# Performance work log

Measured on AMD Instinct MI355X. Metric: run time of the kernel, lower is better.

## Reference

```python
import jax, jax.numpy as jnp
import numpy as np

K = 512   # codebook entries per group (num_embeddings // 4)
D = 128   # dim per group (embedding_dim // 4)
BETA = 0.25


def setup_inputs() -> dict:
    key = jax.random.key(0)
    k0, k1, k2, k3, k4 = jax.random.split(key, 5)
    latents = jax.random.normal(k0, (16, 2048, 512), dtype=jnp.float32)
    scale = 1.0 / K
    w1 = jax.random.uniform(k1, (K, D), dtype=jnp.float32, minval=-scale, maxval=scale)
    w2 = jax.random.uniform(k2, (K, D), dtype=jnp.float32, minval=-scale, maxval=scale)
    w3 = jax.random.uniform(k3, (K, D), dtype=jnp.float32, minval=-scale, maxval=scale)
    w4 = jax.random.uniform(k4, (K, D), dtype=jnp.float32, minval=-scale, maxval=scale)
    return {"latents": latents, "w1": w1, "w2": w2, "w3": w3, "w4": w4}


def _vq(latents, w1, w2, w3, w4):
    B, S, E = latents.shape
    # Slicing [:, :, g*D:(g+1)*D] is equivalent to reshape into groups.
    x = latents.reshape(B, S, 4, D)                    # [B,S,4,D]
    W = jnp.stack([w1, w2, w3, w4], axis=0)            # [4,K,D]
    x_sq = jnp.sum(x * x, axis=-1, keepdims=True)      # [B,S,4,1]
    w_sq = jnp.sum(W * W, axis=-1)                     # [4,K]
    cross = jnp.einsum('bsgd,gkd->bsgk', x, W)         # [B,S,4,K]
    dist = x_sq + w_sq[None, None, :, :] - 2.0 * cross
    idx = jnp.argmin(dist, axis=-1)                    # [B,S,4]
    g_idx = jnp.arange(4)[None, None, :]
    q = W[g_idx, idx]                                  # [B,S,4,D]
    # per-group MSE losses (mean over B,S,D)
    sg = jax.lax.stop_gradient
    commit = jnp.mean((sg(q) - x) ** 2, axis=(0, 1, 3))   # [4]
    embed = jnp.mean((q - sg(x)) ** 2, axis=(0, 1, 3))    # [4]
    vq_loss = jnp.sum(BETA * commit + embed)
    # straight-through estimator
    q_st = x + sg(q - x)
    return q_st.reshape(B, S, E), vq_loss


def reference(latents, w1, w2, w3, w4):
    return _vq(latents, w1, w2, w3, w4)
```

## Files before the change

### kernel.cpp

```cpp
#include <hip/hip_runtime.h>
#include <stdint.h>

typedef __attribute__((ext_vector_type(8))) short short8;
typedef __attribute__((ext_vector_type(4))) float f32x4;

#define BIG 4.0f

static __device__ __forceinline__ short f2bf(float f) {
    union { float f; uint32_t u; } v; v.f = f;
    uint32_t u = v.u;
    return (short)((u + 0x7FFFu + ((u >> 16) & 1u)) >> 16);
}

static __device__ __forceinline__ void gload_lds16(const void* g, void* l) {
    __builtin_amdgcn_global_load_lds(
        (const __attribute__((address_space(1))) unsigned int*)g,
        (__attribute__((address_space(3))) unsigned int*)l, 16, 0, 0);
}


__global__ void vq_prep_kernel(const float* __restrict__ w0, const float* __restrict__ w1,
                               const float* __restrict__ w2, const float* __restrict__ w3,
                               float* __restrict__ ws) {
    int tid = blockIdx.x * 256 + threadIdx.x;
    int code = tid >> 4;
    int u    = tid & 15;
    int g = code >> 9, c = code & 511;
    int nt = c >> 4, lr = c & 15, ks = u >> 2, lh = u & 3;
    const float* wg = (g == 0) ? w0 : (g == 1) ? w1 : (g == 2) ? w2 : w3;
    const float* src = wg + (size_t)c * 128 + u * 8;
    float4 v0 = *(const float4*)(src);
    float4 v1 = *(const float4*)(src + 4);
    float s = v0.x*v0.x + v0.y*v0.y + v0.z*v0.z + v0.w*v0.w
            + v1.x*v1.x + v1.y*v1.y + v1.z*v1.z + v1.w*v1.w;
    short8 b;
    b[0] = f2bf(v0.x); b[1] = f2bf(v0.y); b[2] = f2bf(v0.z); b[3] = f2bf(v0.w);
    b[4] = f2bf(v1.x); b[5] = f2bf(v1.y); b[6] = f2bf(v1.z); b[7] = f2bf(v1.w);
    char* cb = (char*)ws + 65536 + (size_t)g * 131072;
    *(short8*)(cb + (size_t)(((nt * 4 + ks) * 64 + lh * 16 + lr) * 16)) = b;
    s += __shfl_xor(s, 1); s += __shfl_xor(s, 2);
    s += __shfl_xor(s, 4); s += __shfl_xor(s, 8);
    if (u == 0) ws[64 + code] = BIG - 0.5f * s;
}

__global__ __launch_bounds__(512, 2)
void vq_main_kernel(const float* __restrict__ lat,
                    const float* __restrict__ w0, const float* __restrict__ w1,
                    const float* __restrict__ w2, const float* __restrict__ w3,
                    float* __restrict__ out, float* __restrict__ ws) {
    __shared__ __align__(16) short lw[65536];
    __shared__ float lwsq[512];
    __shared__ float slsum[8];

    const int bid   = blockIdx.x;
    const int g     = bid >> 6;
    const int tbase = (bid & 63) * 512;
    const float* wg = (g == 0) ? w0 : (g == 1) ? w1 : (g == 2) ? w2 : w3;
    const char* cbg = (const char*)ws + 65536 + (size_t)g * 131072;

    const int t    = threadIdx.x;
    const int wave = t >> 6;
    const int l    = t & 63;
    const int lr   = l & 15;
    const int lh   = l >> 4;
    const int col  = (l & 31) * 4;
    const uint32_t invlr = 511 - lr;

    lwsq[t] = ws[64 + g * 512 + t];

    {
        const char* gsrc = cbg + wave * 16384 + l * 16;
        char* ldst = (char*)lw + wave * 16384;
        #pragma unroll
        for (int j = 0; j < 16; j++)
            gload_lds16(gsrc + j * 1024, ldst + j * 1024);
    }

    auto load_convert = [&](short8 (&fr)[2][4], float (&xsp)[2], int wt) {
        #pragma unroll
        for (int mt = 0; mt < 2; mt++) {
            int token = wt + mt * 16 + lr;
            const float* xp = lat + (size_t)token * 512 + g * 128 + lh * 8;
            float part = 0.f;
            #pragma unroll
            for (int ks = 0; ks < 4; ks++) {
                float4 v0 = *(const float4*)(xp + ks * 32);
                float4 v1 = *(const float4*)(xp + ks * 32 + 4);
                part += v0.x*v0.x + v0.y*v0.y + v0.z*v0.z + v0.w*v0.w
                      + v1.x*v1.x + v1.y*v1.y + v1.z*v1.z + v1.w*v1.w;
                short8 a;
                a[0] = f2bf(v0.x); a[1] = f2bf(v0.y); a[2] = f2bf(v0.z); a[3] = f2bf(v0.w);
                a[4] = f2bf(v1.x); a[5] = f2bf(v1.y); a[6] = f2bf(v1.z); a[7] = f2bf(v1.w);
                fr[mt][ks] = a;
            }
            part += __shfl_xor(part, 16);
            part += __shfl_xor(part, 32);
            xsp[mt] = part;
        }
    };

    const char* lwb = (const char*)lw + l * 16;

    auto compute = [&](short8 (&af)[2][4], uint32_t (&rk)[8]) {
        short8 p0 = *(const short8*)(lwb);
        short8 p1 = *(const short8*)(lwb + 1024);
        short8 p2 = *(const short8*)(lwb + 2048);
        short8 p3 = *(const short8*)(lwb + 3072);
        float  ph = lwsq[lr];
        #pragma unroll 4
        for (int nt = 0; nt < 32; nt++) {
            short8 c0 = p0, c1 = p1, c2 = p2, c3 = p3;
            float  hn = ph;
            const char* nb = lwb + ((nt + 1) & 31) * 4096;
            p0 = *(const short8*)(nb);
            p1 = *(const short8*)(nb + 1024);
            p2 = *(const short8*)(nb + 2048);
            p3 = *(const short8*)(nb + 3072);
            ph = lwsq[(((nt + 1) & 31) << 4) + lr];
            const uint32_t invc = invlr - (uint32_t)(nt * 16);
            __builtin_amdgcn_s_setprio(1);
            f32x4 acc0 = {hn, hn, hn, hn};
            f32x4 acc1 = {hn, hn, hn, hn};
            acc0 = __builtin_amdgcn_mfma_f32_16x16x32_bf16(af[0][0], c0, acc0, 0, 0, 0);
            acc0 = __builtin_amdgcn_mfma_f32_16x16x32_bf16(af[0][1], c1, acc0, 0, 0, 0);
            acc0 = __builtin_amdgcn_mfma_f32_16x16x32_bf16(af[0][2], c2, acc0, 0, 0, 0);
            acc0 = __builtin_amdgcn_mfma_f32_16x16x32_bf16(af[0][3], c3, acc0, 0, 0, 0);
            acc1 = __builtin_amdgcn_mfma_f32_16x16x32_bf16(af[1][0], c0, acc1, 0, 0, 0);
            acc1 = __builtin_amdgcn_mfma_f32_16x16x32_bf16(af[1][1], c1, acc1, 0, 0, 0);
            acc1 = __builtin_amdgcn_mfma_f32_16x16x32_bf16(af[1][2], c2, acc1, 0, 0, 0);
            acc1 = __builtin_amdgcn_mfma_f32_16x16x32_bf16(af[1][3], c3, acc1, 0, 0, 0);
            __builtin_amdgcn_s_setprio(0);
            #pragma unroll
            for (int r = 0; r < 4; r++) {
                rk[r]     = max(rk[r],     (__float_as_uint(acc0[r]) & 0xFFFFFE00u) | invc);
                rk[4 + r] = max(rk[4 + r], (__float_as_uint(acc1[r]) & 0xFFFFFE00u) | invc);
            }
        }
    };

    auto epilogue = [&](uint32_t (&rk)[8], float (&xsp)[2], int wt, float& acc_lsum) {
        int runidx[8];
        #pragma unroll
        for (int i = 0; i < 8; i++) {
            uint32_t k = rk[i];
            k = max(k, (uint32_t)__shfl_xor((int)k, 1));
            k = max(k, (uint32_t)__shfl_xor((int)k, 2));
            k = max(k, (uint32_t)__shfl_xor((int)k, 4));
            k = max(k, (uint32_t)__shfl_xor((int)k, 8));
            rk[i] = k;
            runidx[i] = 511 - (int)(k & 0x1FFu);
        }
        #pragma unroll
        for (int mt = 0; mt < 2; mt++) {
            #pragma unroll
            for (int r = 0; r < 4; r++) {
                int row = lh * 4 + r;
                float xs = __shfl(xsp[mt], (l & 48) | row);
                float val = __uint_as_float(rk[mt * 4 + r] & 0xFFFFFE00u);
                if (lr == 0) acc_lsum += xs + 2.f * BIG - 2.f * val;
            }
        }
        #pragma unroll
        for (int it = 0; it < 16; it++) {
            const int j0 = it * 2, j1 = it * 2 + 1;
            int idx0 = __shfl(runidx[((j0 >> 4) << 2) | (j0 & 3)], ((j0 >> 2) & 3) << 4);
            int idx1 = __shfl(runidx[((j1 >> 4) << 2) | (j1 & 3)], ((j1 >> 2) & 3) << 4);
            int idx  = (l >= 32) ? idx1 : idx0;
            int tloc = it * 2 + (l >> 5);
            float4 v = *(const float4*)(wg + (size_t)idx * 128 + col);
            *(float4*)(out + (size_t)(wt + tloc) * 512 + g * 128 + col) = v;
        }
    };

    const int wtok = tbase + wave * 64;

    short8 fA[2][4], fB[2][4];
    float  xspA[2], xspB[2];
    uint32_t kA[8], kB[8];
    #pragma unroll
    for (int i = 0; i < 8; i++) { kA[i] = 0u; kB[i] = 0u; }

    load_convert(fA, xspA, wtok);
    __syncthreads();

    float lsum = 0.f;
    compute(fA, kA);

    float4 raw[16];
    #pragma unroll
    for (int mt = 0; mt < 2; mt++) {
        #pragma unroll
        for (int ks = 0; ks < 4; ks++) {
            const float* xp = lat + (size_t)(wtok + 32 + mt * 16 + lr) * 512
                            + g * 128 + lh * 8 + ks * 32;
            raw[mt * 8 + ks * 2]     = *(const float4*)(xp);
            raw[mt * 8 + ks * 2 + 1] = *(const float4*)(xp + 4);
        }
    }

    int runidxA[8];
    #pragma unroll
    for (int i = 0; i < 8; i++) {
        uint32_t k = kA[i];
        k = max(k, (uint32_t)__shfl_xor((int)k, 1));
        k = max(k, (uint32_t)__shfl_xor((int)k, 2));
        k = max(k, (uint32_t)__shfl_xor((int)k, 4));
        k = max(k, (uint32_t)__shfl_xor((int)k, 8));
        kA[i] = k;
        runidxA[i] = 511 - (int)(k & 0x1FFu);
    }
    #pragma unroll
    for (int mt = 0; mt < 2; mt++) {
        #pragma unroll
        for (int r = 0; r < 4; r++) {
            int row = lh * 4 + r;
            float xs = __shfl(xspA[mt], (l & 48) | row);
            float val = __uint_as_float(kA[mt * 4 + r] & 0xFFFFFE00u);
            if (lr == 0) lsum += xs + 2.f * BIG - 2.f * val;
        }
    }
    int widx[16];
    #pragma unroll
    for (int it = 0; it < 16; it++) {
        const int j0 = it * 2, j1 = it * 2 + 1;
        int idx0 = __shfl(runidxA[((j0 >> 4) << 2) | (j0 & 3)], ((j0 >> 2) & 3) << 4);
        int idx1 = __shfl(runidxA[((j1 >> 4) << 2) | (j1 & 3)], ((j1 >> 2) & 3) << 4);
        widx[it] = (l >= 32) ? idx1 : idx0;
    }

    #pragma unroll
    for (int mt = 0; mt < 2; mt++) {
        float part = 0.f;
        #pragma unroll
        for (int ks = 0; ks < 4; ks++) {
            float4 v0 = raw[mt * 8 + ks * 2];
            float4 v1 = raw[mt * 8 + ks * 2 + 1];
            part += v0.x*v0.x + v0.y*v0.y + v0.z*v0.z + v0.w*v0.w
                  + v1.x*v1.x + v1.y*v1.y + v1.z*v1.z + v1.w*v1.w;
            short8 a;
            a[0] = f2bf(v0.x); a[1] = f2bf(v0.y); a[2] = f2bf(v0.z); a[3] = f2bf(v0.w);
            a[4] = f2bf(v1.x); a[5] = f2bf(v1.y); a[6] = f2bf(v1.z); a[7] = f2bf(v1.w);
            fB[mt][ks] = a;
        }
        part += __shfl_xor(part, 16);
        part += __shfl_xor(part, 32);
        xspB[mt] = part;
    }

    {
        short8 p0 = *(const short8*)(lwb);
        short8 p1 = *(const short8*)(lwb + 1024);
        short8 p2 = *(const short8*)(lwb + 2048);
        short8 p3 = *(const short8*)(lwb + 3072);
        float  ph = lwsq[lr];
        float4 vb0, vb1;

#define FUSED_NT(nt)                                                           \
        {                                                                      \
            short8 c0 = p0, c1 = p1, c2 = p2, c3 = p3;                         \
            float  hn = ph;                                                    \
            const char* nb = lwb + (((nt) + 1) & 31) * 4096;                   \
            p0 = *(const short8*)(nb);                                         \
            p1 = *(const short8*)(nb + 1024);                                  \
            p2 = *(const short8*)(nb + 2048);                                  \
            p3 = *(const short8*)(nb + 3072);                                  \
            ph = lwsq[((((nt) + 1) & 31) << 4) + lr];                          \
            const uint32_t invc = invlr - (uint32_t)((nt) * 16);               \
            __builtin_amdgcn_s_setprio(1);                                     \
            f32x4 acc0 = {hn, hn, hn, hn};                                     \
            f32x4 acc1 = {hn, hn, hn, hn};                                     \
            acc0 = __builtin_amdgcn_mfma_f32_16x16x32_bf16(fB[0][0], c0, acc0, 0, 0, 0); \
            acc0 = __builtin_amdgcn_mfma_f32_16x16x32_bf16(fB[0][1], c1, acc0, 0, 0, 0); \
            acc0 = __builtin_amdgcn_mfma_f32_16x16x32_bf16(fB[0][2], c2, acc0, 0, 0, 0); \
            acc0 = __builtin_amdgcn_mfma_f32_16x16x32_bf16(fB[0][3], c3, acc0, 0, 0, 0); \
            acc1 = __builtin_amdgcn_mfma_f32_16x16x32_bf16(fB[1][0], c0, acc1, 0, 0, 0); \
            acc1 = __builtin_amdgcn_mfma_f32_16x16x32_bf16(fB[1][1], c1, acc1, 0, 0, 0); \
            acc1 = __builtin_amdgcn_mfma_f32_16x16x32_bf16(fB[1][2], c2, acc1, 0, 0, 0); \
            acc1 = __builtin_amdgcn_mfma_f32_16x16x32_bf16(fB[1][3], c3, acc1, 0, 0, 0); \
            __builtin_amdgcn_s_setprio(0);                                     \
            kB[0] = max(kB[0], (__float_as_uint(acc0[0]) & 0xFFFFFE00u) | invc); \
            kB[1] = max(kB[1], (__float_as_uint(acc0[1]) & 0xFFFFFE00u) | invc); \
            kB[2] = max(kB[2], (__float_as_uint(acc0[2]) & 0xFFFFFE00u) | invc); \
            kB[3] = max(kB[3], (__float_as_uint(acc0[3]) & 0xFFFFFE00u) | invc); \
            kB[4] = max(kB[4], (__float_as_uint(acc1[0]) & 0xFFFFFE00u) | invc); \
            kB[5] = max(kB[5], (__float_as_uint(acc1[1]) & 0xFFFFFE00u) | invc); \
            kB[6] = max(kB[6], (__float_as_uint(acc1[2]) & 0xFFFFFE00u) | invc); \
            kB[7] = max(kB[7], (__float_as_uint(acc1[3]) & 0xFFFFFE00u) | invc); \
            if (((nt) & 3) == 1) {                                             \
                const int it0 = ((nt) >> 2) * 2;                               \
                vb0 = *(const float4*)(wg + (size_t)widx[it0] * 128 + col);    \
                vb1 = *(const float4*)(wg + (size_t)widx[it0 + 1] * 128 + col);\
            }                                                                  \
            if (((nt) & 3) == 3) {                                             \
                const int it0 = ((nt) >> 2) * 2;                               \
                *(float4*)(out + (size_t)(wtok + it0 * 2 + (l >> 5)) * 512     \
                           + g * 128 + col) = vb0;                             \
                *(float4*)(out + (size_t)(wtok + (it0 + 1) * 2 + (l >> 5)) * 512 \
                           + g * 128 + col) = vb1;                             \
            }                                                                  \
        }
#define FUSED_4(n) FUSED_NT(n) FUSED_NT((n) + 1) FUSED_NT((n) + 2) FUSED_NT((n) + 3)
        FUSED_4(0)  FUSED_4(4)  FUSED_4(8)  FUSED_4(12)
        FUSED_4(16) FUSED_4(20) FUSED_4(24) FUSED_4(28)
#undef FUSED_4
#undef FUSED_NT
    }

    epilogue(kB, xspB, wtok + 32, lsum);

    lsum += __shfl_xor(lsum, 16);
    lsum += __shfl_xor(lsum, 32);
    if (l == 0) slsum[wave] = lsum;
    __syncthreads();
    if (t == 0) {
        float s = 0.f;
        #pragma unroll
        for (int i = 0; i < 8; i++) s += slsum[i];
        ws[4096 + bid] = s;
    }
}

__global__ void vq_finalize_kernel(const float* __restrict__ ws, float* __restrict__ out) {
    __shared__ float s4[4];
    float v = ws[4096 + threadIdx.x];
    #pragma unroll
    for (int m = 1; m < 64; m <<= 1) v += __shfl_xor(v, m);
    if ((threadIdx.x & 63) == 0) s4[threadIdx.x >> 6] = v;
    __syncthreads();
    if (threadIdx.x == 0)
        out[16777216] = 1.25f * (s4[0] + s4[1] + s4[2] + s4[3]) * (1.0f / 4194304.0f);
}

extern "C" void kernel_launch(void* const* d_in, const int* in_sizes, int n_in,
                              void* d_out, int out_size, void* d_ws, size_t ws_size,
                              hipStream_t stream) {
    const float* lat = (const float*)d_in[0];
    const float* w1  = (const float*)d_in[1];
    const float* w2  = (const float*)d_in[2];
    const float* w3  = (const float*)d_in[3];
    const float* w4  = (const float*)d_in[4];
    float* out = (float*)d_out;
    float* ws  = (float*)d_ws;

    vq_prep_kernel<<<128, 256, 0, stream>>>(w1, w2, w3, w4, ws);
    vq_main_kernel<<<256, 512, 0, stream>>>(lat, w1, w2, w3, w4, out, ws);
    vq_finalize_kernel<<<1, 256, 0, stream>>>(ws, out);
}
```

Measured before the change: 40.43 us.

## Rebalance wave pipeline to 48 tokens in phase A and 16 in phase B

Splits each wave's 64 tokens unevenly: the first compute phase now handles three 16-token tiles (48 tokens) with interleaved MFMA chains, and the second phase handles one tile while overlapping the gather/store of the 48 quantized rows. Interleaving three independent accumulator chains is meant to hide MFMA latency and reuse each LDS codebook fragment across more tokens. The fused second phase spreads more output writes over the shorter loop. The cost is higher register pressure from 12 A-fragments, 12 key registers and 24 gather indices, which may lower occupancy or cause spills.

```diff
diff --git a/kernel.cpp b/kernel.cpp
--- a/kernel.cpp
+++ b/kernel.cpp
@@ -76,32 +76,43 @@
             gload_lds16(gsrc + j * 1024, ldst + j * 1024);
     }
 
-    auto load_convert = [&](short8 (&fr)[2][4], float (&xsp)[2], int wt) {
-        #pragma unroll
-        for (int mt = 0; mt < 2; mt++) {
-            int token = wt + mt * 16 + lr;
-            const float* xp = lat + (size_t)token * 512 + g * 128 + lh * 8;
-            float part = 0.f;
-            #pragma unroll
-            for (int ks = 0; ks < 4; ks++) {
-                float4 v0 = *(const float4*)(xp + ks * 32);
-                float4 v1 = *(const float4*)(xp + ks * 32 + 4);
-                part += v0.x*v0.x + v0.y*v0.y + v0.z*v0.z + v0.w*v0.w
-                      + v1.x*v1.x + v1.y*v1.y + v1.z*v1.z + v1.w*v1.w;
-                short8 a;
-                a[0] = f2bf(v0.x); a[1] = f2bf(v0.y); a[2] = f2bf(v0.z); a[3] = f2bf(v0.w);
-                a[4] = f2bf(v1.x); a[5] = f2bf(v1.y); a[6] = f2bf(v1.z); a[7] = f2bf(v1.w);
-                fr[mt][ks] = a;
-            }
-            part += __shfl_xor(part, 16);
-            part += __shfl_xor(part, 32);
-            xsp[mt] = part;
-        }
-    };
-
     const char* lwb = (const char*)lw + l * 16;
-
-    auto compute = [&](short8 (&af)[2][4], uint32_t (&rk)[8]) {
+    const int wtok = tbase + wave * 64;
+
+    short8 fA[3][4];
+    float  xspA[3];
+    #pragma unroll
+    for (int mt = 0; mt < 3; mt++) {
+        int token = wtok + mt * 16 + lr;
+        const float* xp = lat + (size_t)token * 512 + g * 128 + lh * 8;
+        float part = 0.f;
+        #pragma unroll
+        for (int ks = 0; ks < 4; ks++) {
+            float4 v0 = *(const float4*)(xp + ks * 32);
+            float4 v1 = *(const float4*)(xp + ks * 32 + 4);
+            part += v0.x*v0.x + v0.y*v0.y + v0.z*v0.z + v0.w*v0.w
+                  + v1.x*v1.x + v1.y*v1.y + v1.z*v1.z + v1.w*v1.w;
+            short8 a;
+            a[0] = f2bf(v0.x); a[1] = f2bf(v0.y); a[2] = f2bf(v0.z); a[3] = f2bf(v0.w);
+            a[4] = f2bf(v1.x); a[5] = f2bf(v1.y); a[6] = f2bf(v1.z); a[7] = f2bf(v1.w);
+            fA[mt][ks] = a;
+        }
+        part += __shfl_xor(part, 16);
+        part += __shfl_xor(part, 32);
+        xspA[mt] = part;
+    }
+
+    uint32_t kA[12], kB[4];
+    #pragma unroll
+    for (int i = 0; i < 12; i++) kA[i] = 0u;
+    #pragma unroll
+    for (int i = 0; i < 4; i++) kB[i] = 0u;
+
+    __syncthreads();
+
+    float lsum = 0.f;
+
+    {
         short8 p0 = *(const short8*)(lwb);
         short8 p1 = *(const short8*)(lwb + 1024);
         short8 p2 = *(const short8*)(lwb + 2048);
@@ -121,86 +132,42 @@
             __builtin_amdgcn_s_setprio(1);
             f32x4 acc0 = {hn, hn, hn, hn};
             f32x4 acc1 = {hn, hn, hn, hn};
-            acc0 = __builtin_amdgcn_mfma_f32_16x16x32_bf16(af[0][0], c0, acc0, 0, 0, 0);
-            acc0 = __builtin_amdgcn_mfma_f32_16x16x32_bf16(af[0][1], c1, acc0, 0, 0, 0);
-            acc0 = __builtin_amdgcn_mfma_f32_16x16x32_bf16(af[0][2], c2, acc0, 0, 0, 0);
-            acc0 = __builtin_amdgcn_mfma_f32_16x16x32_bf16(af[0][3], c3, acc0, 0, 0, 0);
-            acc1 = __builtin_amdgcn_mfma_f32_16x16x32_bf16(af[1][0], c0, acc1, 0, 0, 0);
-            acc1 = __builtin_amdgcn_mfma_f32_16x16x32_bf16(af[1][1], c1, acc1, 0, 0, 0);
-            acc1 = __builtin_amdgcn_mfma_f32_16x16x32_bf16(af[1][2], c2, acc1, 0, 0, 0);
-            acc1 = __builtin_amdgcn_mfma_f32_16x16x32_bf16(af[1][3], c3, acc1, 0, 0, 0);
+            f32x4 acc2 = {hn, hn, hn, hn};
+            acc0 = __builtin_amdgcn_mfma_f32_16x16x32_bf16(fA[0][0], c0, acc0, 0, 0, 0);
+            acc1 = __builtin_amdgcn_mfma_f32_16x16x32_bf16(fA[1][0], c0, acc1, 0, 0, 0);
+            acc2 = __builtin_amdgcn_mfma_f32_16x16x32_bf16(fA[2][0], c0, acc2, 0, 0, 0);
+            acc0 = __builtin_amdgcn_mfma_f32_16x16x32_bf16(fA[0][1], c1, acc0, 0, 0, 0);
+            acc1 = __builtin_amdgcn_mfma_f32_16x16x32_bf16(fA[1][1], c1, acc1, 0, 0, 0);
+            acc2 = __builtin_amdgcn_mfma_f32_16x16x32_bf16(fA[2][1], c1, acc2, 0, 0, 0);
+            acc0 = __builtin_amdgcn_mfma_f32_16x16x32_bf16(fA[0][2], c2, acc0, 0, 0, 0);
+            acc1 = __builtin_amdgcn_mfma_f32_16x16x32_bf16(fA[1][2], c2, acc1, 0, 0, 0);
+            acc2 = __builtin_amdgcn_mfma_f32_16x16x32_bf16(fA[2][2], c2, acc2, 0, 0, 0);
+            acc0 = __builtin_amdgcn_mfma_f32_16x16x32_bf16(fA[0][3], c3, acc0, 0, 0, 0);
+            acc1 = __builtin_amdgcn_mfma_f32_16x16x32_bf16(fA[1][3], c3, acc1, 0, 0, 0);
+            acc2 = __builtin_amdgcn_mfma_f32_16x16x32_bf16(fA[2][3], c3, acc2, 0, 0, 0);
             __builtin_amdgcn_s_setprio(0);
             #pragma unroll
             for (int r = 0; r < 4; r++) {
-                rk[r]     = max(rk[r],     (__float_as_uint(acc0[r]) & 0xFFFFFE00u) | invc);
-                rk[4 + r] = max(rk[4 + r], (__float_as_uint(acc1[r]) & 0xFFFFFE00u) | invc);
+                kA[r]     = max(kA[r],     (__float_as_uint(acc0[r]) & 0xFFFFFE00u) | invc);
+                kA[4 + r] = max(kA[4 + r], (__float_as_uint(acc1[r]) & 0xFFFFFE00u) | invc);
+                kA[8 + r] = max(kA[8 + r], (__float_as_uint(acc2[r]) & 0xFFFFFE00u) | invc);
             }
         }
-    };
-
-    auto epilogue = [&](uint32_t (&rk)[8], float (&xsp)[2], int wt, float& acc_lsum) {
-        int runidx[8];
-        #pragma unroll
-        for (int i = 0; i < 8; i++) {
-            uint32_t k = rk[i];
-            k = max(k, (uint32_t)__shfl_xor((int)k, 1));
-            k = max(k, (uint32_t)__shfl_xor((int)k, 2));
-            k = max(k, (uint32_t)__shfl_xor((int)k, 4));
-            k = max(k, (uint32_t)__shfl_xor((int)k, 8));
-            rk[i] = k;
-            runidx[i] = 511 - (int)(k & 0x1FFu);
-        }
-        #pragma unroll
-        for (int mt = 0; mt < 2; mt++) {
-            #pragma unroll
-            for (int r = 0; r < 4; r++) {
-                int row = lh * 4 + r;
-                float xs = __shfl(xsp[mt], (l & 48) | row);
-                float val = __uint_as_float(rk[mt * 4 + r] & 0xFFFFFE00u);
-                if (lr == 0) acc_lsum += xs + 2.f * BIG - 2.f * val;
-            }
-        }
-        #pragma unroll
-        for (int it = 0; it < 16; it++) {
-            const int j0 = it * 2, j1 = it * 2 + 1;
-            int idx0 = __shfl(runidx[((j0 >> 4) << 2) | (j0 & 3)], ((j0 >> 2) & 3) << 4);
-            int idx1 = __shfl(runidx[((j1 >> 4) << 2) | (j1 & 3)], ((j1 >> 2) & 3) << 4);
-            int idx  = (l >= 32) ? idx1 : idx0;
-            int tloc = it * 2 + (l >> 5);
-            float4 v = *(const float4*)(wg + (size_t)idx * 128 + col);
-            *(float4*)(out + (size_t)(wt + tloc) * 512 + g * 128 + col) = v;
-        }
-    };
-
-    const int wtok = tbase + wave * 64;
-
-    short8 fA[2][4], fB[2][4];
-    float  xspA[2], xspB[2];
-    uint32_t kA[8], kB[8];
-    #pragma unroll
-    for (int i = 0; i < 8; i++) { kA[i] = 0u; kB[i] = 0u; }
-
-    load_convert(fA, xspA, wtok);
-    __syncthreads();
-
-    float lsum = 0.f;
-    compute(fA, kA);
-
-    float4 raw[16];
-    #pragma unroll
-    for (int mt = 0; mt < 2; mt++) {
+    }
+
+    float4 raw[8];
+    {
+        const float* xp = lat + (size_t)(wtok + 48 + lr) * 512 + g * 128 + lh * 8;
         #pragma unroll
         for (int ks = 0; ks < 4; ks++) {
-            const float* xp = lat + (size_t)(wtok + 32 + mt * 16 + lr) * 512
-                            + g * 128 + lh * 8 + ks * 32;
-            raw[mt * 8 + ks * 2]     = *(const float4*)(xp);
-            raw[mt * 8 + ks * 2 + 1] = *(const float4*)(xp + 4);
-        }
-    }
-
-    int runidxA[8];
-    #pragma unroll
-    for (int i = 0; i < 8; i++) {
+            raw[ks * 2]     = *(const float4*)(xp + ks * 32);
+            raw[ks * 2 + 1] = *(const float4*)(xp + ks * 32 + 4);
+        }
+    }
+
+    int runidxA[12];
+    #pragma unroll
+    for (int i = 0; i < 12; i++) {
         uint32_t k = kA[i];
         k = max(k, (uint32_t)__shfl_xor((int)k, 1));
         k = max(k, (uint32_t)__shfl_xor((int)k, 2));
@@ -210,7 +177,7 @@
         runidxA[i] = 511 - (int)(k & 0x1FFu);
     }
     #pragma unroll
-    for (int mt = 0; mt < 2; mt++) {
+    for (int mt = 0; mt < 3; mt++) {
         #pragma unroll
         for (int r = 0; r < 4; r++) {
             int row = lh * 4 + r;
@@ -219,32 +186,33 @@
             if (lr == 0) lsum += xs + 2.f * BIG - 2.f * val;
         }
     }
-    int widx[16];
-    #pragma unroll
-    for (int it = 0; it < 16; it++) {
+    int widx[24];
+    #pragma unroll
+    for (int it = 0; it < 24; it++) {
         const int j0 = it * 2, j1 = it * 2 + 1;
         int idx0 = __shfl(runidxA[((j0 >> 4) << 2) | (j0 & 3)], ((j0 >> 2) & 3) << 4);
         int idx1 = __shfl(runidxA[((j1 >> 4) << 2) | (j1 & 3)], ((j1 >> 2) & 3) << 4);
         widx[it] = (l >= 32) ? idx1 : idx0;
     }
 
-    #pragma unroll
-    for (int mt = 0; mt < 2; mt++) {
+    short8 fB[4];
+    float  xspB;
+    {
         float part = 0.f;
         #pragma unroll
         for (int ks = 0; ks < 4; ks++) {
-            float4 v0 = raw[mt * 8 + ks * 2];
-            float4 v1 = raw[mt * 8 + ks * 2 + 1];
+            float4 v0 = raw[ks * 2];
+            float4 v1 = raw[ks * 2 + 1];
             part += v0.x*v0.x + v0.y*v0.y + v0.z*v0.z + v0.w*v0.w
                   + v1.x*v1.x + v1.y*v1.y + v1.z*v1.z + v1.w*v1.w;
             short8 a;
             a[0] = f2bf(v0.x); a[1] = f2bf(v0.y); a[2] = f2bf(v0.z); a[3] = f2bf(v0.w);
             a[4] = f2bf(v1.x); a[5] = f2bf(v1.y); a[6] = f2bf(v1.z); a[7] = f2bf(v1.w);
-            fB[mt][ks] = a;
+            fB[ks] = a;
         }
         part += __shfl_xor(part, 16);
         part += __shfl_xor(part, 32);
-        xspB[mt] = part;
+        xspB = part;
     }
 
     {
@@ -253,7 +221,7 @@
         short8 p2 = *(const short8*)(lwb + 2048);
         short8 p3 = *(const short8*)(lwb + 3072);
         float  ph = lwsq[lr];
-        float4 vb0, vb1;
+        float4 vb0, vb1, vb2;
 
 #define FUSED_NT(nt)                                                           \
         {                                                                      \
@@ -267,36 +235,30 @@
             ph = lwsq[((((nt) + 1) & 31) << 4) + lr];                          \
             const uint32_t invc = invlr - (uint32_t)((nt) * 16);               \
             __builtin_amdgcn_s_setprio(1);                                     \
-            f32x4 acc0 = {hn, hn, hn, hn};                                     \
-            f32x4 acc1 = {hn, hn, hn, hn};                                     \
-            acc0 = __builtin_amdgcn_mfma_f32_16x16x32_bf16(fB[0][0], c0, acc0, 0, 0, 0); \
-            acc0 = __builtin_amdgcn_mfma_f32_16x16x32_bf16(fB[0][1], c1, acc0, 0, 0, 0); \
-            acc0 = __builtin_amdgcn_mfma_f32_16x16x32_bf16(fB[0][2], c2, acc0, 0, 0, 0); \
-            acc0 = __builtin_amdgcn_mfma_f32_16x16x32_bf16(fB[0][3], c3, acc0, 0, 0, 0); \
-            acc1 = __builtin_amdgcn_mfma_f32_16x16x32_bf16(fB[1][0], c0, acc1, 0, 0, 0); \
-            acc1 = __builtin_amdgcn_mfma_f32_16x16x32_bf16(fB[1][1], c1, acc1, 0, 0, 0); \
-            acc1 = __builtin_amdgcn_mfma_f32_16x16x32_bf16(fB[1][2], c2, acc1, 0, 0, 0); \
-            acc1 = __builtin_amdgcn_mfma_f32_16x16x32_bf16(fB[1][3], c3, acc1, 0, 0, 0); \
+            f32x4 acc = {hn, hn, hn, hn};                                      \
+            acc = __builtin_amdgcn_mfma_f32_16x16x32_bf16(fB[0], c0, acc, 0, 0, 0); \
+            acc = __builtin_amdgcn_mfma_f32_16x16x32_bf16(fB[1], c1, acc, 0, 0, 0); \
+            acc = __builtin_amdgcn_mfma_f32_16x16x32_bf16(fB[2], c2, acc, 0, 0, 0); \
+            acc = __builtin_amdgcn_mfma_f32_16x16x32_bf16(fB[3], c3, acc, 0, 0, 0); \
             __builtin_amdgcn_s_setprio(0);                                     \
-            kB[0] = max(kB[0], (__float_as_uint(acc0[0]) & 0xFFFFFE00u) | invc); \
-            kB[1] = max(kB[1], (__float_as_uint(acc0[1]) & 0xFFFFFE00u) | invc); \
-            kB[2] = max(kB[2], (__float_as_uint(acc0[2]) & 0xFFFFFE00u) | invc); \
-            kB[3] = max(kB[3], (__float_as_uint(acc0[3]) & 0xFFFFFE00u) | invc); \
-            kB[4] = max(kB[4], (__float_as_uint(acc1[0]) & 0xFFFFFE00u) | invc); \
-            kB[5] = max(kB[5], (__float_as_uint(acc1[1]) & 0xFFFFFE00u) | invc); \
-            kB[6] = max(kB[6], (__float_as_uint(acc1[2]) & 0xFFFFFE00u) | invc); \
-            kB[7] = max(kB[7], (__float_as_uint(acc1[3]) & 0xFFFFFE00u) | invc); \
+            kB[0] = max(kB[0], (__float_as_uint(acc[0]) & 0xFFFFFE00u) | invc); \
+            kB[1] = max(kB[1], (__float_as_uint(acc[1]) & 0xFFFFFE00u) | invc); \
+            kB[2] = max(kB[2], (__float_as_uint(acc[2]) & 0xFFFFFE00u) | invc); \
+            kB[3] = max(kB[3], (__float_as_uint(acc[3]) & 0xFFFFFE00u) | invc); \
             if (((nt) & 3) == 1) {                                             \
-                const int it0 = ((nt) >> 2) * 2;                               \
+                const int it0 = ((nt) >> 2) * 3;                               \
                 vb0 = *(const float4*)(wg + (size_t)widx[it0] * 128 + col);    \
                 vb1 = *(const float4*)(wg + (size_t)widx[it0 + 1] * 128 + col);\
+                vb2 = *(const float4*)(wg + (size_t)widx[it0 + 2] * 128 + col);\
             }                                                                  \
             if (((nt) & 3) == 3) {                                             \
-                const int it0 = ((nt) >> 2) * 2;                               \
+                const int it0 = ((nt) >> 2) * 3;                               \
                 *(float4*)(out + (size_t)(wtok + it0 * 2 + (l >> 5)) * 512     \
                            + g * 128 + col) = vb0;                             \
                 *(float4*)(out + (size_t)(wtok + (it0 + 1) * 2 + (l >> 5)) * 512 \
                            + g * 128 + col) = vb1;                             \
+                *(float4*)(out + (size_t)(wtok + (it0 + 2) * 2 + (l >> 5)) * 512 \
+                           + g * 128 + col) = vb2;                             \
             }                                                                  \
         }
 #define FUSED_4(n) FUSED_NT(n) FUSED_NT((n) + 1) FUSED_NT((n) + 2) FUSED_NT((n) + 3)
@@ -306,7 +268,36 @@
 #undef FUSED_NT
     }
 
-    epilogue(kB, xspB, wtok + 32, lsum);
+    {
+        int runidxB[4];
+        #pragma unroll
+        for (int i = 0; i < 4; i++) {
+            uint32_t k = kB[i];
+            k = max(k, (uint32_t)__shfl_xor((int)k, 1));
+            k = max(k, (uint32_t)__shfl_xor((int)k, 2));
+            k = max(k, (uint32_t)__shfl_xor((int)k, 4));
+            k = max(k, (uint32_t)__shfl_xor((int)k, 8));
+            kB[i] = k;
+            runidxB[i] = 511 - (int)(k & 0x1FFu);
+        }
+        #pragma unroll
+        for (int r = 0; r < 4; r++) {
+            int row = lh * 4 + r;
+            float xs = __shfl(xspB, (l & 48) | row);
+            float val = __uint_as_float(kB[r] & 0xFFFFFE00u);
+            if (lr == 0) lsum += xs + 2.f * BIG - 2.f * val;
+        }
+        #pragma unroll
+        for (int it = 0; it < 8; it++) {
+            const int j0 = it * 2, j1 = it * 2 + 1;
+            int idx0 = __shfl(runidxB[j0 & 3], ((j0 >> 2) & 3) << 4);
+            int idx1 = __shfl(runidxB[j1 & 3], ((j1 >> 2) & 3) << 4);
+            int idx  = (l >= 32) ? idx1 : idx0;
+            int tloc = 48 + it * 2 + (l >> 5);
+            float4 v = *(const float4*)(wg + (size_t)idx * 128 + col);
+            *(float4*)(out + (size_t)(wtok + tloc) * 512 + g * 128 + col) = v;
+        }
+    }
 
     lsum += __shfl_xor(lsum, 16);
     lsum += __shfl_xor(lsum, 32);
```

Measured after the change: 40.99 us. No clear change (+1.4%).
